# Kernel tuning notes

Measured on AMD Instinct MI355X. Metric: run time of the kernel, lower is better.

## Reference

```python
import jax, jax.numpy as jnp
import numpy as np
from jax import lax

# pywt Wavelet('db4') decomposition filters
DEC_LO = jnp.array([-0.010597401784997278, 0.032883011666982945, 0.030841381835986965,
                    -0.18703481171888114, -0.02798376941698385, 0.6308807679295904,
                    0.7148465705525415, 0.23037781330885523], dtype=jnp.float32)
DEC_HI = jnp.array([-0.23037781330885523, 0.7148465705525415, -0.6308807679295904,
                    -0.02798376941698385, 0.18703481171888114, 0.030841381835986965,
                    -0.032883011666982945, -0.010597401784997278], dtype=jnp.float32)


def dwt_level(x, lo, hi):
    # single-level pywt dwt, mode='symmetric', along last axis
    f = lo.shape[0]
    p = f - 1
    pad = [(0, 0)] * (x.ndim - 1) + [(p, p)]
    xe = jnp.pad(x, pad, mode='symmetric')[..., 1:]  # offset 1 matches pywt phase
    lead = x.shape[:-1]
    xin = xe.reshape(-1, 1, xe.shape[-1])            # [N,1,L]
    filt = jnp.stack([lo[::-1], hi[::-1]])[:, None, :]  # flip: true convolution, [2,1,f]
    out = lax.conv_general_dilated(xin, filt, (2,), 'VALID')  # [N,2,floor((n+f-1)/2)]
    cA = out[:, 0].reshape(lead + (-1,))
    cD = out[:, 1].reshape(lead + (-1,))
    return cA, cD


def wavedec4(x):
    # pywt.wavedec(x,'db4',level=4) concatenated: [cA4,cD4,cD3,cD2,cD1]
    details = []
    a = x
    for _ in range(4):
        a, d = dwt_level(a, DEC_LO, DEC_HI)
        details.append(d)
    return jnp.concatenate([a] + details[::-1], axis=-1)


def lstm_last(xs, w_ih, w_hh, b_ih, b_hh):
    # torch LSTM (gate order i,f,g,o); returns last timestep hidden state
    B, T, _ = xs.shape
    H = w_hh.shape[1]
    h0 = jnp.zeros((B, H), xs.dtype)
    c0 = jnp.zeros((B, H), xs.dtype)
    b = b_ih + b_hh

    def step(carry, x_t):
        h, c = carry
        gates = x_t @ w_ih.T + h @ w_hh.T + b
        i, f, g, o = jnp.split(gates, 4, axis=-1)
        c = jax.nn.sigmoid(f) * c + jax.nn.sigmoid(i) * jnp.tanh(g)
        h = jax.nn.sigmoid(o) * jnp.tanh(c)
        return (h, c), None

    (h, _), _ = lax.scan(step, (h0, c0), jnp.swapaxes(xs, 0, 1))
    return h


def setup_inputs() -> dict:
    key = jax.random.key(0)
    ks = jax.random.split(key, 9)
    B, S, T = 256, 1024, 21
    return {
        'x': jax.random.normal(ks[0], (B, S, T), jnp.float32),
        'conv_w': jax.random.normal(ks[1], (64, 78, 3), jnp.float32) * 0.06,
        'conv_b': jax.random.normal(ks[2], (64,), jnp.float32) * 0.06,
        'w_ih': jax.random.normal(ks[3], (128, 64), jnp.float32) * 0.12,
        'w_hh': jax.random.normal(ks[4], (128, 32), jnp.float32) * 0.17,
        'b_ih': jax.random.normal(ks[5], (128,), jnp.float32) * 0.17,
        'b_hh': jax.random.normal(ks[6], (128,), jnp.float32) * 0.17,
        'fc_w': jax.random.normal(ks[7], (1, 32), jnp.float32) * 0.17,
        'fc_b': jax.random.normal(ks[8], (1,), jnp.float32) * 0.17,
    }


def reference(x, conv_w, conv_b, w_ih, w_hh, b_ih, b_hh, fc_w, fc_b):
    freq = jnp.abs(jnp.fft.rfft(x, axis=2))          # [B,S,11]
    tf = wavedec4(x)                                 # [B,S,46]
    combined = jnp.concatenate([x, freq, tf], axis=2)  # [B,S,78]
    combined = jnp.swapaxes(combined, 1, 2)          # [B,78,S]
    y = lax.conv_general_dilated(combined, conv_w, (1,), [(1, 1)]) + conv_b[None, :, None]
    y = jax.nn.relu(y)
    B, C, S = y.shape
    y = y.reshape(B, C, S // 2, 2).max(axis=-1)      # max_pool1d(k=2,s=2)
    y = jnp.transpose(y, (0, 2, 1))                  # [B,S//2,64]
    h = lstm_last(y, w_ih, w_hh, b_ih, b_hh)         # [B,32]
    return h @ fc_w.T + fc_b                         # [B,1]
```

## Files before the change

kernel.cpp:

```cpp
#include <hip/hip_runtime.h>
#include <math.h>

typedef _Float16 half8 __attribute__((ext_vector_type(8)));
typedef float floatx16 __attribute__((ext_vector_type(16)));
typedef float float2v __attribute__((ext_vector_type(2)));

constexpr float L2E = 1.4426950408889634f;

constexpr float DLO[8] = {-0.010597401784997278f, 0.032883011666982945f, 0.030841381835986965f,
                          -0.18703481171888114f, -0.02798376941698385f, 0.6308807679295904f,
                          0.7148465705525415f, 0.23037781330885523f};
constexpr float DHI[8] = {-0.23037781330885523f, 0.7148465705525415f, -0.6308807679295904f,
                          -0.02798376941698385f, 0.18703481171888114f, 0.030841381835986965f,
                          -0.032883011666982945f, -0.010597401784997278f};

constexpr float CT21[21] = {
  1.0f,          0.95557281f,  0.82623877f,  0.62348980f,  0.36534102f,  0.07473009f,
  -0.22252093f, -0.5f,        -0.73305187f, -0.90096887f, -0.98883083f,
  -0.98883083f, -0.90096887f, -0.73305187f, -0.5f,        -0.22252093f,
  0.07473009f,   0.36534102f,  0.62348980f,  0.82623877f,  0.95557281f};
constexpr float ST21[21] = {
  0.0f,          0.29475517f,  0.56332006f,  0.78183148f,  0.93087375f,  0.99720380f,
  0.97492791f,   0.86602540f,  0.68017274f,  0.43388374f,  0.14904227f,
  -0.14904227f, -0.43388374f, -0.68017274f, -0.86602540f, -0.97492791f,
  -0.99720380f, -0.93087375f, -0.78183148f, -0.56332006f, -0.29475517f};

template<int N>
__device__ __forceinline__ void dwt_step(const float* in, float* a, float* d) {
  constexpr int NO = (N + 7) / 2;
#pragma unroll
  for (int i = 0; i < NO; i++) {
    float sa = 0.f, sd = 0.f;
#pragma unroll
    for (int j = 0; j < 8; j++) {
      int rel = 2 * i + j - 6;
      int idx = (rel < 0) ? (-rel - 1) : ((rel >= N) ? (2 * N - rel - 1) : rel);
      float v = in[idx];
      sa = fmaf(v, DLO[7 - j], sa);
      sd = fmaf(v, DHI[7 - j], sd);
    }
    a[i] = sa;
    d[i] = sd;
  }
}

__device__ __forceinline__ void gload_lds16(const void* g, void* l) {
  __builtin_amdgcn_global_load_lds(
      (const __attribute__((address_space(1))) unsigned int*)g,
      (__attribute__((address_space(3))) unsigned int*)l, 16, 0, 0);
}

__global__ __launch_bounds__(256) void features_kernel(const float* __restrict__ x,
                                                       _Float16* __restrict__ comb_t) {
  __shared__ __align__(16) char smem[256 * 104 * 2];
  float* xl = (float*)smem;
  _Float16* hb = (_Float16*)smem;

  const int tid = threadIdx.x;
  const int g0 = blockIdx.x * 256;
  for (int idx = tid; idx < 256 * 21; idx += 256) xl[idx] = x[g0 * 21 + idx];
  __syncthreads();

  float xx[21];
#pragma unroll
  for (int t = 0; t < 21; t++) xx[t] = xl[tid * 21 + t];
  __syncthreads();

  __align__(16) _Float16 hrow[88];
#pragma unroll
  for (int i = 78; i < 88; i++) hrow[i] = (_Float16)0.f;

#pragma unroll
  for (int t = 0; t < 21; t++) hrow[t] = (_Float16)xx[t];

#pragma unroll
  for (int k = 0; k < 11; k++) {
    float re = 0.f, im = 0.f;
#pragma unroll
    for (int t = 0; t < 21; t++) {
      const int m = (k * t) % 21;
      re = fmaf(xx[t], CT21[m], re);
      im = fmaf(xx[t], ST21[m], im);
    }
    hrow[21 + k] = (_Float16)sqrtf(re * re + im * im);
  }

  float a1[14], d1[14];
  dwt_step<21>(xx, a1, d1);
#pragma unroll
  for (int i = 0; i < 14; i++) hrow[64 + i] = (_Float16)d1[i];
  float a2[10], d2[10];
  dwt_step<14>(a1, a2, d2);
#pragma unroll
  for (int i = 0; i < 10; i++) hrow[54 + i] = (_Float16)d2[i];
  float a3[8], d3[8];
  dwt_step<10>(a2, a3, d3);
#pragma unroll
  for (int i = 0; i < 8; i++) hrow[46 + i] = (_Float16)d3[i];
  float a4[7], d4[7];
  dwt_step<8>(a3, a4, d4);
#pragma unroll
  for (int i = 0; i < 7; i++) {
    hrow[32 + i] = (_Float16)a4[i];
    hrow[39 + i] = (_Float16)d4[i];
  }

  {
    uint4* hv = (uint4*)&hb[tid * 104];
    const uint4* srcv = (const uint4*)hrow;
#pragma unroll
    for (int i = 0; i < 11; i++) hv[i] = srcv[i];
  }
  __syncthreads();

  uint4* dstv = (uint4*)(comb_t + (size_t)g0 * 88);
#pragma unroll
  for (int it = 0; it < 11; it++) {
    const int k = it * 256 + tid;
    const int s = k / 11;
    const int e8 = k - s * 11;
    dstv[k] = *(const uint4*)&hb[s * 104 + e8 * 8];
  }
}

__global__ __launch_bounds__(256) void wprep_kernel(const float* __restrict__ cw,
                                                    const float* __restrict__ w_ih,
                                                    const float* __restrict__ b_ih,
                                                    const float* __restrict__ b_hh,
                                                    _Float16* __restrict__ WbT,
                                                    _Float16* __restrict__ wih16,
                                                    float* __restrict__ biasI) {
  int idx = blockIdx.x * 256 + threadIdx.x;
  if (idx < 64 * 264) {
    int o = idx / 264, k = idx - o * 264;
    float v = 0.f;
    if (k < 240) {
      int dk = k / 80, c = k - dk * 80;
      if (c < 78) v = cw[o * 234 + c * 3 + dk];
    }
    WbT[idx] = (_Float16)v;
  } else if (idx < 16896 + 8192) {
    int j = idx - 16896;
    wih16[j] = (_Float16)(L2E * w_ih[j]);
  } else if (idx < 16896 + 8192 + 128) {
    int g = idx - 16896 - 8192;
    int p = ((g & 63) << 1) | (g >> 6);
    biasI[p] = L2E * (b_ih[g] + b_hh[g]);
  }
}

__global__ __launch_bounds__(256, 2) void conv_proj_kernel(const _Float16* __restrict__ comb_t,
                                                           const _Float16* __restrict__ WbT,
                                                           const float* __restrict__ cbias,
                                                           const _Float16* __restrict__ wih16,
                                                           const float* __restrict__ biasI,
                                                           float* __restrict__ Xp) {
  __shared__ __align__(16) char smem[61184];
  _Float16* At = (_Float16*)smem;
  _Float16* Bt = (_Float16*)(smem + 24576);
  _Float16* yt = (_Float16*)smem;
  _Float16* wl = (_Float16*)(smem + 9216);
  float* biasl = (float*)(smem + 27648);
  float* Xpt   = (float*)(smem + 28160);
  float* bl    = (float*)(smem + 60928);

  const int tid = threadIdx.x;
  const int b = blockIdx.y;
  const int s0 = blockIdx.x * 128;
  const int T0 = blockIdx.x * 64;

  {
    const char* srcA = (const char*)(comb_t + (size_t)((b << 10) + s0 - 1) * 88);
#pragma unroll
    for (int i = 0; i < 6; i++) {
      const int idx = i * 256 + tid;
      const int cidx = (idx < 1430) ? idx : 1429;
      gload_lds16(srcA + (size_t)cidx * 16, (char*)At + (size_t)idx * 16);
    }
    const char* srcB = (const char*)WbT;
#pragma unroll
    for (int i = 0; i < 8; i++) {
      const int idx = i * 256 + tid;
      gload_lds16(srcB + (size_t)idx * 16, (char*)Bt + (size_t)idx * 16);
    }
    if (tid < 64)
      gload_lds16(srcB + (size_t)(2048 + tid) * 16, (char*)Bt + (size_t)(2048 + tid) * 16);
  }
  if (tid < 64) bl[tid] = cbias[tid];
  __syncthreads();
  if (s0 == 0 && tid < 88) At[tid] = (_Float16)0.f;
  if (s0 == 896 && tid < 88) At[129 * 88 + tid] = (_Float16)0.f;
  __syncthreads();

  const int wave = tid >> 6, lane = tid & 63;
  const int ml = lane & 31;
  const int kg = lane >> 5;
  const int am = wave * 32 + ml;

  floatx16 acc0 = {};
  floatx16 acc1 = {};
#pragma unroll
  for (int ks = 0; ks < 15; ks++) {
    const int kb = ks * 16 + kg * 8;
    const int dk = (kb >= 160) ? 2 : ((kb >= 80) ? 1 : 0);
    const int c = kb - dk * 80;
    half8 av = *(const half8*)&At[(am + dk) * 88 + c];
    half8 bv0 = *(const half8*)&Bt[ml * 264 + kb];
    half8 bv1 = *(const half8*)&Bt[(32 + ml) * 264 + kb];
    acc0 = __builtin_amdgcn_mfma_f32_32x32x16_f16(av, bv0, acc0, 0, 0, 0);
    acc1 = __builtin_amdgcn_mfma_f32_32x32x16_f16(av, bv1, acc1, 0, 0, 0);
  }

  const float b0 = bl[ml], b1 = bl[32 + ml];
  float v0s[8], v1s[8];
#pragma unroll
  for (int p = 0; p < 8; p++) {
    v0s[p] = fmaxf(fmaxf(acc0[2 * p], acc0[2 * p + 1]) + b0, 0.f);
    v1s[p] = fmaxf(fmaxf(acc1[2 * p], acc1[2 * p + 1]) + b1, 0.f);
  }

  __syncthreads();

#pragma unroll
  for (int p = 0; p < 8; p++) {
    const int toff = (p & 1) + ((p >> 1) << 2);
    const int t = wave * 16 + (kg << 1) + toff;
    yt[t * 72 + ml] = (_Float16)v0s[p];
    yt[t * 72 + 32 + ml] = (_Float16)v1s[p];
  }
  for (int i = tid; i < 2048; i += 256) {
    int g = i >> 4, c4 = i & 15;
    *(uint2*)(wl + g * 72 + c4 * 4) = *(const uint2*)(wih16 + g * 64 + c4 * 4);
  }
  if (tid < 128) biasl[tid] = biasI[tid];
  __syncthreads();

  const int tm = wave & 1, tn0 = (wave >> 1) * 2;
  floatx16 pa0 = {};
  floatx16 pa1 = {};
#pragma unroll
  for (int kq = 0; kq < 4; kq++) {
    const int k0 = kq * 16 + kg * 8;
    half8 av = *(const half8*)&yt[(tm * 32 + ml) * 72 + k0];
    half8 bv0 = *(const half8*)&wl[(tn0 * 32 + ml) * 72 + k0];
    half8 bv1 = *(const half8*)&wl[((tn0 + 1) * 32 + ml) * 72 + k0];
    pa0 = __builtin_amdgcn_mfma_f32_32x32x16_f16(av, bv0, pa0, 0, 0, 0);
    pa1 = __builtin_amdgcn_mfma_f32_32x32x16_f16(av, bv1, pa1, 0, 0, 0);
  }

  {
    const int g0i = tn0 * 32 + ml;
    const int p0 = ((g0i & 63) << 1) | (g0i >> 6);
    const int g1i = (tn0 + 1) * 32 + ml;
    const int p1 = ((g1i & 63) << 1) | (g1i >> 6);
#pragma unroll
    for (int reg = 0; reg < 16; reg++) {
      const int row = (reg & 3) + 8 * (reg >> 2) + 4 * kg;
      const int m = tm * 32 + row;
      Xpt[m * 128 + p0] = pa0[reg];
      Xpt[m * 128 + p1] = pa1[reg];
    }
  }
  __syncthreads();

  float* xpg = Xp + ((size_t)b * 512 + T0) * 128;
  for (int i = tid; i < 2048; i += 256) {
    const int r = i >> 5, c4 = (i & 31) << 2;
    float4 v = *(float4*)&Xpt[r * 128 + c4];
    float4 bb = *(float4*)&biasl[c4];
    v.x += bb.x; v.y += bb.y; v.z += bb.z; v.w += bb.w;
    *(float4*)&xpg[r * 128 + c4] = v;
  }
}

__device__ __forceinline__ float bcast_lane(float v, int k) {
  return __uint_as_float(__builtin_amdgcn_readlane(__float_as_uint(v), k));
}

#if __has_builtin(__builtin_amdgcn_exp2f)
#define EXP2F __builtin_amdgcn_exp2f
#else
#define EXP2F exp2f
#endif

#if __has_builtin(__builtin_amdgcn_permlane32_swap)
__device__ __forceinline__ float swap_half(float x) {
  auto r = __builtin_amdgcn_permlane32_swap(__float_as_uint(x), __float_as_uint(x),
                                            false, false);
  return __uint_as_float(r[1]);
}
#else
__device__ __forceinline__ float swap_half(float x) { return __shfl_down(x, 32); }
#endif

__device__ __forceinline__ void lstm_step(float& h, float& c, float2v xg,
                                          const float* __restrict__ wA,
                                          const float* __restrict__ wB, bool lo) {
  float hs[32];
#pragma unroll
  for (int k = 0; k < 32; k++) hs[k] = bcast_lane(h, k);

  float aA0 = xg.x, aA1 = 0.f, aB0 = xg.y, aB1 = 0.f;
#pragma unroll
  for (int k = 0; k < 32; k += 2) {
    aA0 = fmaf(hs[k], wA[k], aA0);
    aB0 = fmaf(hs[k], wB[k], aB0);
    aA1 = fmaf(hs[k + 1], wA[k + 1], aA1);
    aB1 = fmaf(hs[k + 1], wB[k + 1], aB1);
  }
  const float gA = aA0 + aA1;
  const float gB = aB0 + aB1;

  float sA = __builtin_amdgcn_rcpf(1.0f + EXP2F(-gA));

  float argB = lo ? (gB + gB) : (-gB);
  float rB = __builtin_amdgcn_rcpf(EXP2F(argB) + 1.0f);
  float sB = lo ? fmaf(-2.f, rB, 1.f) : rB;

  float fv = swap_half(sA);
  float ov = swap_half(sB);
  c = fmaf(fv, c, sA * sB);
  float rc = __builtin_amdgcn_rcpf(EXP2F(c * (2.f * L2E)) + 1.0f);
  float ov2 = ov + ov;
  h = fmaf(-ov2, rc, ov);
}

__global__ __launch_bounds__(64, 1)
__attribute__((amdgpu_waves_per_eu(1, 1)))
void lstm_fc_kernel(const float* __restrict__ Xp,
                    const float* __restrict__ w_hh,
                    const float* __restrict__ fc_w,
                    const float* __restrict__ fc_b,
                    float* __restrict__ out) {
  const int b = blockIdx.x;
  const int L = threadIdx.x;
  const bool lo = (L < 32);

  float wA[32], wB[32];
  {
    const float4* rA = (const float4*)(w_hh + L * 32);
    const float4* rB = (const float4*)(w_hh + (L + 64) * 32);
#pragma unroll
    for (int q = 0; q < 8; q++) {
      float4 a4 = rA[q], b4 = rB[q];
      wA[4 * q + 0] = L2E * a4.x; wA[4 * q + 1] = L2E * a4.y;
      wA[4 * q + 2] = L2E * a4.z; wA[4 * q + 3] = L2E * a4.w;
      wB[4 * q + 0] = L2E * b4.x; wB[4 * q + 1] = L2E * b4.y;
      wB[4 * q + 2] = L2E * b4.z; wB[4 * q + 3] = L2E * b4.w;
    }
  }

  const float* xp = Xp + (size_t)b * 512 * 128;
  float h = 0.f, c = 0.f;

  float2v p2[4];
#pragma unroll
  for (int u = 0; u < 4; u++) p2[u] = *(const float2v*)&xp[u * 128 + 2 * L];

  for (int t0 = 0; t0 < 512; t0 += 4) {
    float2v c2[4];
#pragma unroll
    for (int u = 0; u < 4; u++) c2[u] = p2[u];
    if (t0 + 4 < 512) {
#pragma unroll
      for (int u = 0; u < 4; u++)
        p2[u] = *(const float2v*)&xp[(t0 + 4 + u) * 128 + 2 * L];
    }
#pragma unroll
    for (int u = 0; u < 4; u++) lstm_step(h, c, c2[u], wA, wB, lo);
  }

  float v = lo ? h * fc_w[L & 31] : 0.f;
#pragma unroll
  for (int off = 32; off > 0; off >>= 1) v += __shfl_down(v, off);
  if (L == 0) out[b] = v + fc_b[0];
}

extern "C" void kernel_launch(void* const* d_in, const int* in_sizes, int n_in,
                              void* d_out, int out_size, void* d_ws, size_t ws_size,
                              hipStream_t stream) {
  const float* x      = (const float*)d_in[0];
  const float* conv_w = (const float*)d_in[1];
  const float* conv_b = (const float*)d_in[2];
  const float* w_ih   = (const float*)d_in[3];
  const float* w_hh   = (const float*)d_in[4];
  const float* b_ih   = (const float*)d_in[5];
  const float* b_hh   = (const float*)d_in[6];
  const float* fc_w   = (const float*)d_in[7];
  const float* fc_b   = (const float*)d_in[8];
  float* out = (float*)d_out;

  char* wsb = (char*)d_ws;
  _Float16* comb_t = (_Float16*)(wsb + 256);
  float*    Xp     = (float*)(wsb + 256 + 46137344);
  _Float16* WbT    = (_Float16*)(wsb + 256 + 46137344 + 67108864);
  _Float16* wih16  = (_Float16*)(wsb + 256 + 46137344 + 67108864 + 33792);
  float*    biasI  = (float*)(wsb + 256 + 46137344 + 67108864 + 33792 + 16384);

  wprep_kernel<<<dim3(99), dim3(256), 0, stream>>>(conv_w, w_ih, b_ih, b_hh,
                                                   WbT, wih16, biasI);
  features_kernel<<<dim3(1024), dim3(256), 0, stream>>>(x, comb_t);
  conv_proj_kernel<<<dim3(8, 256), dim3(256), 0, stream>>>(comb_t, WbT, conv_b,
                                                           wih16, biasI, Xp);
  lstm_fc_kernel<<<dim3(256), dim3(64), 0, stream>>>(Xp, w_hh, fc_w, fc_b, out);
}
```

Measured before the change: 230.0 us.

## Fuse feature extraction into conv_proj kernel, dropping comb_t intermediate

The separate features kernel and its 46MB fp16 intermediate buffer are removed. Each conv_proj block now computes the FFT-magnitude and wavelet features for its 130 rows (including halo rows) directly from x into LDS. This removes one kernel launch and a global write plus read of the combined features. In exchange, halo rows are computed twice, only 130 of 256 threads do the feature work, and x is read with uncoalesced per-thread strided loads.

```diff
diff --git a/kernel.cpp b/kernel.cpp
--- a/kernel.cpp
+++ b/kernel.cpp
@@ -50,23 +50,12 @@
       (__attribute__((address_space(3))) unsigned int*)l, 16, 0, 0);
 }
 
-__global__ __launch_bounds__(256) void features_kernel(const float* __restrict__ x,
-                                                       _Float16* __restrict__ comb_t) {
-  __shared__ __align__(16) char smem[256 * 104 * 2];
-  float* xl = (float*)smem;
-  _Float16* hb = (_Float16*)smem;
-
-  const int tid = threadIdx.x;
-  const int g0 = blockIdx.x * 256;
-  for (int idx = tid; idx < 256 * 21; idx += 256) xl[idx] = x[g0 * 21 + idx];
-  __syncthreads();
-
+__device__ __forceinline__ void feature_row(const float* __restrict__ xr,
+                                            _Float16* hrow) {
   float xx[21];
 #pragma unroll
-  for (int t = 0; t < 21; t++) xx[t] = xl[tid * 21 + t];
-  __syncthreads();
-
-  __align__(16) _Float16 hrow[88];
+  for (int t = 0; t < 21; t++) xx[t] = xr[t];
+
 #pragma unroll
   for (int i = 78; i < 88; i++) hrow[i] = (_Float16)0.f;
 
@@ -103,23 +92,6 @@
   for (int i = 0; i < 7; i++) {
     hrow[32 + i] = (_Float16)a4[i];
     hrow[39 + i] = (_Float16)d4[i];
-  }
-
-  {
-    uint4* hv = (uint4*)&hb[tid * 104];
-    const uint4* srcv = (const uint4*)hrow;
-#pragma unroll
-    for (int i = 0; i < 11; i++) hv[i] = srcv[i];
-  }
-  __syncthreads();
-
-  uint4* dstv = (uint4*)(comb_t + (size_t)g0 * 88);
-#pragma unroll
-  for (int it = 0; it < 11; it++) {
-    const int k = it * 256 + tid;
-    const int s = k / 11;
-    const int e8 = k - s * 11;
-    dstv[k] = *(const uint4*)&hb[s * 104 + e8 * 8];
   }
 }
 
@@ -149,7 +121,7 @@
   }
 }
 
-__global__ __launch_bounds__(256, 2) void conv_proj_kernel(const _Float16* __restrict__ comb_t,
+__global__ __launch_bounds__(256, 2) void conv_proj_kernel(const float* __restrict__ x,
                                                            const _Float16* __restrict__ WbT,
                                                            const float* __restrict__ cbias,
                                                            const _Float16* __restrict__ wih16,
@@ -170,13 +142,6 @@
   const int T0 = blockIdx.x * 64;
 
   {
-    const char* srcA = (const char*)(comb_t + (size_t)((b << 10) + s0 - 1) * 88);
-#pragma unroll
-    for (int i = 0; i < 6; i++) {
-      const int idx = i * 256 + tid;
-      const int cidx = (idx < 1430) ? idx : 1429;
-      gload_lds16(srcA + (size_t)cidx * 16, (char*)At + (size_t)idx * 16);
-    }
     const char* srcB = (const char*)WbT;
 #pragma unroll
     for (int i = 0; i < 8; i++) {
@@ -187,9 +152,21 @@
       gload_lds16(srcB + (size_t)(2048 + tid) * 16, (char*)Bt + (size_t)(2048 + tid) * 16);
   }
   if (tid < 64) bl[tid] = cbias[tid];
-  __syncthreads();
-  if (s0 == 0 && tid < 88) At[tid] = (_Float16)0.f;
-  if (s0 == 896 && tid < 88) At[129 * 88 + tid] = (_Float16)0.f;
+
+  if (tid < 130) {
+    const int s = s0 - 1 + tid;
+    __align__(16) _Float16 hrow[88];
+    if (s < 0 || s > 1023) {
+#pragma unroll
+      for (int i = 0; i < 88; i++) hrow[i] = (_Float16)0.f;
+    } else {
+      feature_row(x + ((size_t)(b << 10) + s) * 21, hrow);
+    }
+    uint4* dst = (uint4*)&At[tid * 88];
+    const uint4* src = (const uint4*)hrow;
+#pragma unroll
+    for (int i = 0; i < 11; i++) dst[i] = src[i];
+  }
   __syncthreads();
 
   const int wave = tid >> 6, lane = tid & 63;
@@ -391,16 +368,14 @@
   float* out = (float*)d_out;
 
   char* wsb = (char*)d_ws;
-  _Float16* comb_t = (_Float16*)(wsb + 256);
-  float*    Xp     = (float*)(wsb + 256 + 46137344);
-  _Float16* WbT    = (_Float16*)(wsb + 256 + 46137344 + 67108864);
-  _Float16* wih16  = (_Float16*)(wsb + 256 + 46137344 + 67108864 + 33792);
-  float*    biasI  = (float*)(wsb + 256 + 46137344 + 67108864 + 33792 + 16384);
+  float*    Xp    = (float*)wsb;
+  _Float16* WbT   = (_Float16*)(wsb + 67108864);
+  _Float16* wih16 = (_Float16*)(wsb + 67108864 + 33792);
+  float*    biasI = (float*)(wsb + 67108864 + 33792 + 16384);
 
   wprep_kernel<<<dim3(99), dim3(256), 0, stream>>>(conv_w, w_ih, b_ih, b_hh,
                                                    WbT, wih16, biasI);
-  features_kernel<<<dim3(1024), dim3(256), 0, stream>>>(x, comb_t);
-  conv_proj_kernel<<<dim3(8, 256), dim3(256), 0, stream>>>(comb_t, WbT, conv_b,
+  conv_proj_kernel<<<dim3(8, 256), dim3(256), 0, stream>>>(x, WbT, conv_b,
                                                            wih16, biasI, Xp);
   lstm_fc_kernel<<<dim3(256), dim3(64), 0, stream>>>(Xp, w_hh, fc_w, fc_b, out);
 }
```

Result: faster. 224.8 us (-2.3%).
